# Performance work log

Hardware: AMD Instinct MI355X
Metric: run time of the kernel (lower is better)

## Reference

```python
import jax, jax.numpy as jnp
import numpy as np

N = 12288       # number of edge-triangle incidences
D_IN = 2        # input_dim
D_K = 8         # d_k
H1 = 32
H2 = 16
N_EDGES = 6144  # number of segments for scatter_softmax
N_TRI = 4096


def _layernorm(x, g, b, eps=1e-5):
    mu = jnp.mean(x, axis=-1, keepdims=True)
    var = jnp.mean((x - mu) ** 2, axis=-1, keepdims=True)
    return (x - mu) / jnp.sqrt(var + eps) * g + b


def _rmsnorm(x, w, eps=1e-6):
    rms = jnp.sqrt(jnp.mean(x ** 2, axis=-1, keepdims=True))
    return x / (rms + eps) * w


def setup_inputs() -> dict:
    key = jax.random.key(0)
    ks = jax.random.split(key, 16)

    def lin(k, out_d, in_d):
        k1, k2 = jax.random.split(k)
        bound = 1.0 / np.sqrt(in_d)
        W = jax.random.uniform(k1, (out_d, in_d), jnp.float32, -bound, bound)
        b = jax.random.uniform(k2, (out_d,), jnp.float32, -bound, bound)
        return W, b

    Wq, bq = lin(ks[0], D_K, D_IN)
    Wk, bk = lin(ks[1], D_K, D_IN)
    Wv, bv = lin(ks[2], D_K, D_IN)
    W1, b1 = lin(ks[3], H1, D_K)    # Linear(d_k, 32)
    Wr, br = lin(ks[4], H1, H1)     # ResBlock Linear(32, 32)
    W2, b2 = lin(ks[5], H2, H1)     # Linear(32, 16)
    W3, b3 = lin(ks[6], 1, H2)      # Linear(16, 1)

    return {
        "edge_features": jax.random.normal(ks[7], (N, D_IN), jnp.float32),
        "edge_ids_all": jax.random.randint(ks[8], (N,), 0, N_EDGES, jnp.int32),
        "triangle_ids_all": jax.random.randint(ks[9], (N,), 0, N_TRI, jnp.int32),
        "Wq": Wq, "bq": bq, "Wk": Wk, "bk": bk, "Wv": Wv, "bv": bv,
        "W1": W1, "b1": b1,
        "ln1_g": jnp.ones((H1,), jnp.float32), "ln1_b": jnp.zeros((H1,), jnp.float32),
        "rms_w": jnp.ones((H1,), jnp.float32),
        "Wr": Wr, "br": br,
        "ln2_g": jnp.ones((H1,), jnp.float32), "ln2_b": jnp.zeros((H1,), jnp.float32),
        "W2": W2, "b2": b2, "W3": W3, "b3": b3,
    }


def reference(edge_features, edge_ids_all, triangle_ids_all,
              Wq, bq, Wk, bk, Wv, bv,
              W1, b1, ln1_g, ln1_b, rms_w, Wr, br, ln2_g, ln2_b,
              W2, b2, W3, b3):
    q = edge_features @ Wq.T + bq          # [N, d_k]
    k = edge_features @ Wk.T + bk
    v = edge_features @ Wv.T + bv

    scores = (q @ k.T) / np.sqrt(D_K).astype(np.float32)   # [N, N]
    mask = triangle_ids_all[:, None] == triangle_ids_all[None, :]
    scores = jnp.where(mask, scores, -jnp.inf)
    attn = jax.nn.softmax(scores, axis=1)                   # row softmax
    attended = attn @ v                                     # [N, d_k]

    # attention_mlp
    h = _layernorm(attended @ W1.T + b1, ln1_g, ln1_b)
    h = jax.nn.gelu(h, approximate=False)
    h = h + jax.nn.relu(_rmsnorm(h, rms_w) @ Wr.T + br)     # ResBlock
    h = _layernorm(h, ln2_g, ln2_b)
    h = jax.nn.gelu(h @ W2.T + b2, approximate=False)
    logits = (h @ W3.T + b3)[:, 0]                          # [N]

    # scatter_softmax over edge_ids segments
    seg_max = jax.ops.segment_max(logits, edge_ids_all, num_segments=N_EDGES)
    seg_max = jnp.where(jnp.isfinite(seg_max), seg_max, 0.0)
    e = jnp.exp(logits - seg_max[edge_ids_all])
    seg_sum = jax.ops.segment_sum(e, edge_ids_all, num_segments=N_EDGES)
    weights = e / seg_sum[edge_ids_all]
    return weights
```

## Files before the change

### kernel.cpp

```cpp
#include <hip/hip_runtime.h>
#include <math.h>

#define N_INC   12288
#define N_EDGES 6144
#define N_TRI   4096

__device__ __forceinline__ unsigned enc_f(float f) {
    int b = __float_as_int(f);
    return (b >= 0) ? (unsigned(b) | 0x80000000u) : ~unsigned(b);
}
__device__ __forceinline__ float dec_f(unsigned u) {
    int b = (u & 0x80000000u) ? int(u & 0x7FFFFFFFu) : int(~u);
    return __int_as_float(b);
}

__device__ __forceinline__ float gelu_exact(float x) {
    return 0.5f * x * (1.0f + erff(x * 0.70710678118654752f));
}

__global__ void k_qkv(const float* __restrict__ ef, const int* __restrict__ tri,
                      const float* __restrict__ Wq, const float* __restrict__ bq,
                      const float* __restrict__ Wk, const float* __restrict__ bk,
                      const float* __restrict__ Wv, const float* __restrict__ bv,
                      float* __restrict__ q, float* __restrict__ k, float* __restrict__ v,
                      int* __restrict__ counts) {
    int i = blockIdx.x * blockDim.x + threadIdx.x;
    if (i >= N_INC) return;
    float x0 = ef[i * 2], x1 = ef[i * 2 + 1];
#pragma unroll
    for (int d = 0; d < 8; d++) {
        q[i * 8 + d] = Wq[d * 2] * x0 + Wq[d * 2 + 1] * x1 + bq[d];
        k[i * 8 + d] = Wk[d * 2] * x0 + Wk[d * 2 + 1] * x1 + bk[d];
        v[i * 8 + d] = Wv[d * 2] * x0 + Wv[d * 2 + 1] * x1 + bv[d];
    }
    atomicAdd(&counts[tri[i]], 1);
}

__global__ void k_scan(const int* __restrict__ counts,
                       int* __restrict__ offsets, int* __restrict__ cursor) {
    __shared__ int lds[1024];
    int t = threadIdx.x;
    int c0 = counts[t * 4 + 0], c1 = counts[t * 4 + 1];
    int c2 = counts[t * 4 + 2], c3 = counts[t * 4 + 3];
    int s = c0 + c1 + c2 + c3;
    lds[t] = s;
    __syncthreads();
    for (int off = 1; off < 1024; off <<= 1) {
        int val = (t >= off) ? lds[t - off] : 0;
        __syncthreads();
        lds[t] += val;
        __syncthreads();
    }
    int base = lds[t] - s;
    int o0 = base, o1 = base + c0, o2 = o1 + c1, o3 = o2 + c2;
    offsets[t * 4 + 0] = o0; offsets[t * 4 + 1] = o1;
    offsets[t * 4 + 2] = o2; offsets[t * 4 + 3] = o3;
    cursor[t * 4 + 0] = o0;  cursor[t * 4 + 1] = o1;
    cursor[t * 4 + 2] = o2;  cursor[t * 4 + 3] = o3;
    if (t == 1023) offsets[4096] = lds[1023];
}

__global__ void k_fill(const int* __restrict__ tri, int* __restrict__ cursor,
                       int* __restrict__ list) {
    int i = blockIdx.x * blockDim.x + threadIdx.x;
    if (i >= N_INC) return;
    int pos = atomicAdd(&cursor[tri[i]], 1);
    list[pos] = i;
}

__global__ void __launch_bounds__(64)
k_main(const float* __restrict__ q, const float* __restrict__ k, const float* __restrict__ v,
       const int* __restrict__ tri, const int* __restrict__ eid,
       const int* __restrict__ offsets, const int* __restrict__ list,
       const float* __restrict__ W1, const float* __restrict__ b1,
       const float* __restrict__ ln1g, const float* __restrict__ ln1b,
       const float* __restrict__ rmsw,
       const float* __restrict__ Wr, const float* __restrict__ br,
       const float* __restrict__ ln2g, const float* __restrict__ ln2b,
       const float* __restrict__ W2, const float* __restrict__ b2,
       const float* __restrict__ W3, const float* __restrict__ b3,
       float* __restrict__ logits, unsigned* __restrict__ segmax) {
    int i = blockIdx.x * blockDim.x + threadIdx.x;
    if (i >= N_INC) return;

    float qi[8];
#pragma unroll
    for (int d = 0; d < 8; d++) qi[d] = q[i * 8 + d];

    int t = tri[i];
    int s0 = offsets[t], s1 = offsets[t + 1];

    float m = -1e30f, l = 0.f, acc[8];
#pragma unroll
    for (int d = 0; d < 8; d++) acc[d] = 0.f;

    for (int p = s0; p < s1; p++) {
        int j = list[p];
        float sc = 0.f;
#pragma unroll
        for (int d = 0; d < 8; d++) sc += qi[d] * k[j * 8 + d];
        sc *= 0.35355339059327373f;
        float nm = fmaxf(m, sc);
        float scale = expf(m - nm);
        float w = expf(sc - nm);
        l = l * scale + w;
#pragma unroll
        for (int d = 0; d < 8; d++) acc[d] = acc[d] * scale + w * v[j * 8 + d];
        m = nm;
    }
    float inv_l = 1.f / l;
    float att[8];
#pragma unroll
    for (int d = 0; d < 8; d++) att[d] = acc[d] * inv_l;

    float h[32];
#pragma unroll
    for (int o = 0; o < 32; o++) {
        float a = b1[o];
#pragma unroll
        for (int d = 0; d < 8; d++) a += W1[o * 8 + d] * att[d];
        h[o] = a;
    }
    {
        float mu = 0.f;
#pragma unroll
        for (int o = 0; o < 32; o++) mu += h[o];
        mu *= (1.f / 32.f);
        float var = 0.f;
#pragma unroll
        for (int o = 0; o < 32; o++) { float d = h[o] - mu; var += d * d; }
        var *= (1.f / 32.f);
        float is = 1.f / sqrtf(var + 1e-5f);
#pragma unroll
        for (int o = 0; o < 32; o++) h[o] = (h[o] - mu) * is * ln1g[o] + ln1b[o];
    }
#pragma unroll
    for (int o = 0; o < 32; o++) h[o] = gelu_exact(h[o]);
    {
        float ss = 0.f;
#pragma unroll
        for (int o = 0; o < 32; o++) ss += h[o] * h[o];
        float rms = sqrtf(ss * (1.f / 32.f));
        float ir = 1.f / (rms + 1e-6f);
        float hn[32];
#pragma unroll
        for (int o = 0; o < 32; o++) hn[o] = h[o] * ir * rmsw[o];
#pragma unroll
        for (int o = 0; o < 32; o++) {
            float a = br[o];
#pragma unroll
            for (int in = 0; in < 32; in++) a += Wr[o * 32 + in] * hn[in];
            h[o] += fmaxf(a, 0.f);
        }
    }
    {
        float mu = 0.f;
#pragma unroll
        for (int o = 0; o < 32; o++) mu += h[o];
        mu *= (1.f / 32.f);
        float var = 0.f;
#pragma unroll
        for (int o = 0; o < 32; o++) { float d = h[o] - mu; var += d * d; }
        var *= (1.f / 32.f);
        float is = 1.f / sqrtf(var + 1e-5f);
#pragma unroll
        for (int o = 0; o < 32; o++) h[o] = (h[o] - mu) * is * ln2g[o] + ln2b[o];
    }
    float h2[16];
#pragma unroll
    for (int o = 0; o < 16; o++) {
        float a = b2[o];
#pragma unroll
        for (int in = 0; in < 32; in++) a += W2[o * 32 + in] * h[in];
        h2[o] = gelu_exact(a);
    }
    float lg = b3[0];
#pragma unroll
    for (int in = 0; in < 16; in++) lg += W3[in] * h2[in];

    logits[i] = lg;
    atomicMax(&segmax[eid[i]], enc_f(lg));
}

__global__ void k_exp(const float* __restrict__ logits, const int* __restrict__ eid,
                      const unsigned* __restrict__ segmax, float* __restrict__ ebuf,
                      float* __restrict__ segsum) {
    int i = blockIdx.x * blockDim.x + threadIdx.x;
    if (i >= N_INC) return;
    float sm = dec_f(segmax[eid[i]]);
    float ex = expf(logits[i] - sm);
    ebuf[i] = ex;
    atomicAdd(&segsum[eid[i]], ex);
}

__global__ void k_final(const float* __restrict__ ebuf, const int* __restrict__ eid,
                        const float* __restrict__ segsum, float* __restrict__ out) {
    int i = blockIdx.x * blockDim.x + threadIdx.x;
    if (i >= N_INC) return;
    out[i] = ebuf[i] / segsum[eid[i]];
}

extern "C" void kernel_launch(void* const* d_in, const int* in_sizes, int n_in,
                              void* d_out, int out_size, void* d_ws, size_t ws_size,
                              hipStream_t stream) {
    const float* ef   = (const float*)d_in[0];
    const int*   eid  = (const int*)d_in[1];
    const int*   tri  = (const int*)d_in[2];
    const float* Wq   = (const float*)d_in[3];  const float* bq = (const float*)d_in[4];
    const float* Wk   = (const float*)d_in[5];  const float* bk = (const float*)d_in[6];
    const float* Wv   = (const float*)d_in[7];  const float* bv = (const float*)d_in[8];
    const float* W1   = (const float*)d_in[9];  const float* b1 = (const float*)d_in[10];
    const float* ln1g = (const float*)d_in[11]; const float* ln1b = (const float*)d_in[12];
    const float* rmsw = (const float*)d_in[13];
    const float* Wr   = (const float*)d_in[14]; const float* br = (const float*)d_in[15];
    const float* ln2g = (const float*)d_in[16]; const float* ln2b = (const float*)d_in[17];
    const float* W2   = (const float*)d_in[18]; const float* b2 = (const float*)d_in[19];
    const float* W3   = (const float*)d_in[20]; const float* b3 = (const float*)d_in[21];

    float* ws     = (float*)d_ws;
    float* q      = ws;
    float* kk     = q + N_INC * 8;
    float* vv     = kk + N_INC * 8;
    float* logits = vv + N_INC * 8;
    float* ebuf   = logits + N_INC;
    float* segsum = ebuf + N_INC;
    unsigned* segmax = (unsigned*)(segsum + N_EDGES);
    int* counts   = (int*)(segmax + N_EDGES);
    int* offsets  = counts + N_TRI;
    int* cursor   = offsets + N_TRI + 1;
    int* list     = cursor + N_TRI;

    hipMemsetAsync(segsum, 0, (size_t)(2 * N_EDGES + N_TRI) * sizeof(int), stream);

    const int B = 256;
    const int G = (N_INC + B - 1) / B;

    k_qkv<<<G, B, 0, stream>>>(ef, tri, Wq, bq, Wk, bk, Wv, bv, q, kk, vv, counts);
    k_scan<<<1, 1024, 0, stream>>>(counts, offsets, cursor);
    k_fill<<<G, B, 0, stream>>>(tri, cursor, list);
    k_main<<<(N_INC + 63) / 64, 64, 0, stream>>>(q, kk, vv, tri, eid, offsets, list,
                                                 W1, b1, ln1g, ln1b, rmsw, Wr, br,
                                                 ln2g, ln2b, W2, b2, W3, b3,
                                                 logits, segmax);
    k_exp<<<G, B, 0, stream>>>(logits, eid, segmax, ebuf, segsum);
    k_final<<<G, B, 0, stream>>>(ebuf, eid, segsum, (float*)d_out);
}
```

Before: 144.5 us.

## Fuse pipeline into one cooperative kernel with fixed-capacity triangle/edge buckets

Replaces the six-kernel pipeline (QKV, scan, fill, main, exp, final) plus memset with a single cooperative kernel that uses grid-wide syncs between phases. The prefix-scan CSR build is replaced by fixed-capacity buckets per triangle and per edge, filled with atomics. The scatter softmax becomes a per-edge gather pass, which removes the atomicMax and atomicAdd passes. This cuts launch overhead and intermediate buffers. The trade-offs are grid-sync cost, fewer CUs in use (48 blocks), and silent truncation if any segment exceeds the bucket capacity.

```diff
diff --git a/kernel.cpp b/kernel.cpp
--- a/kernel.cpp
+++ b/kernel.cpp
@@ -1,247 +1,199 @@
 #include <hip/hip_runtime.h>
+#include <hip/hip_cooperative_groups.h>
 #include <math.h>
+
+namespace cg = cooperative_groups;
 
 #define N_INC   12288
 #define N_EDGES 6144
 #define N_TRI   4096
+#define CAP_T   32
+#define CAP_E   16
+#define BLK     256
+#define GRD     48
 
-__device__ __forceinline__ unsigned enc_f(float f) {
-    int b = __float_as_int(f);
-    return (b >= 0) ? (unsigned(b) | 0x80000000u) : ~unsigned(b);
-}
-__device__ __forceinline__ float dec_f(unsigned u) {
-    int b = (u & 0x80000000u) ? int(u & 0x7FFFFFFFu) : int(~u);
-    return __int_as_float(b);
-}
+struct Params {
+    const float* ef; const int* eid; const int* tri;
+    const float *Wq, *bq, *Wk, *bk, *Wv, *bv;
+    const float *W1, *b1, *ln1g, *ln1b, *rmsw, *Wr, *br, *ln2g, *ln2b, *W2, *b2, *W3, *b3;
+    float* out;
+    float *kbuf, *vbuf, *logits;
+    int *tri_cnt, *tri_bkt, *edge_cnt, *edge_bkt;
+};
 
 __device__ __forceinline__ float gelu_exact(float x) {
     return 0.5f * x * (1.0f + erff(x * 0.70710678118654752f));
 }
 
-__global__ void k_qkv(const float* __restrict__ ef, const int* __restrict__ tri,
-                      const float* __restrict__ Wq, const float* __restrict__ bq,
-                      const float* __restrict__ Wk, const float* __restrict__ bk,
-                      const float* __restrict__ Wv, const float* __restrict__ bv,
-                      float* __restrict__ q, float* __restrict__ k, float* __restrict__ v,
-                      int* __restrict__ counts) {
-    int i = blockIdx.x * blockDim.x + threadIdx.x;
-    if (i >= N_INC) return;
-    float x0 = ef[i * 2], x1 = ef[i * 2 + 1];
-#pragma unroll
-    for (int d = 0; d < 8; d++) {
-        q[i * 8 + d] = Wq[d * 2] * x0 + Wq[d * 2 + 1] * x1 + bq[d];
-        k[i * 8 + d] = Wk[d * 2] * x0 + Wk[d * 2 + 1] * x1 + bk[d];
-        v[i * 8 + d] = Wv[d * 2] * x0 + Wv[d * 2 + 1] * x1 + bv[d];
-    }
-    atomicAdd(&counts[tri[i]], 1);
-}
+__global__ void __launch_bounds__(BLK)
+fused_kernel(Params p) {
+    cg::grid_group grid = cg::this_grid();
+    const int gid = blockIdx.x * BLK + threadIdx.x;
 
-__global__ void k_scan(const int* __restrict__ counts,
-                       int* __restrict__ offsets, int* __restrict__ cursor) {
-    __shared__ int lds[1024];
-    int t = threadIdx.x;
-    int c0 = counts[t * 4 + 0], c1 = counts[t * 4 + 1];
-    int c2 = counts[t * 4 + 2], c3 = counts[t * 4 + 3];
-    int s = c0 + c1 + c2 + c3;
-    lds[t] = s;
-    __syncthreads();
-    for (int off = 1; off < 1024; off <<= 1) {
-        int val = (t >= off) ? lds[t - off] : 0;
-        __syncthreads();
-        lds[t] += val;
-        __syncthreads();
-    }
-    int base = lds[t] - s;
-    int o0 = base, o1 = base + c0, o2 = o1 + c1, o3 = o2 + c2;
-    offsets[t * 4 + 0] = o0; offsets[t * 4 + 1] = o1;
-    offsets[t * 4 + 2] = o2; offsets[t * 4 + 3] = o3;
-    cursor[t * 4 + 0] = o0;  cursor[t * 4 + 1] = o1;
-    cursor[t * 4 + 2] = o2;  cursor[t * 4 + 3] = o3;
-    if (t == 1023) offsets[4096] = lds[1023];
-}
-
-__global__ void k_fill(const int* __restrict__ tri, int* __restrict__ cursor,
-                       int* __restrict__ list) {
-    int i = blockIdx.x * blockDim.x + threadIdx.x;
-    if (i >= N_INC) return;
-    int pos = atomicAdd(&cursor[tri[i]], 1);
-    list[pos] = i;
-}
-
-__global__ void __launch_bounds__(64)
-k_main(const float* __restrict__ q, const float* __restrict__ k, const float* __restrict__ v,
-       const int* __restrict__ tri, const int* __restrict__ eid,
-       const int* __restrict__ offsets, const int* __restrict__ list,
-       const float* __restrict__ W1, const float* __restrict__ b1,
-       const float* __restrict__ ln1g, const float* __restrict__ ln1b,
-       const float* __restrict__ rmsw,
-       const float* __restrict__ Wr, const float* __restrict__ br,
-       const float* __restrict__ ln2g, const float* __restrict__ ln2b,
-       const float* __restrict__ W2, const float* __restrict__ b2,
-       const float* __restrict__ W3, const float* __restrict__ b3,
-       float* __restrict__ logits, unsigned* __restrict__ segmax) {
-    int i = blockIdx.x * blockDim.x + threadIdx.x;
-    if (i >= N_INC) return;
+    if (gid < N_TRI)   p.tri_cnt[gid]  = 0;
+    if (gid < N_EDGES) p.edge_cnt[gid] = 0;
+    grid.sync();
 
     float qi[8];
+    if (gid < N_INC) {
+        float x0 = p.ef[gid * 2], x1 = p.ef[gid * 2 + 1];
 #pragma unroll
-    for (int d = 0; d < 8; d++) qi[d] = q[i * 8 + d];
+        for (int d = 0; d < 8; d++) {
+            qi[d]               = p.Wq[d * 2] * x0 + p.Wq[d * 2 + 1] * x1 + p.bq[d];
+            p.kbuf[gid * 8 + d] = p.Wk[d * 2] * x0 + p.Wk[d * 2 + 1] * x1 + p.bk[d];
+            p.vbuf[gid * 8 + d] = p.Wv[d * 2] * x0 + p.Wv[d * 2 + 1] * x1 + p.bv[d];
+        }
+        int t = p.tri[gid];
+        int s = atomicAdd(&p.tri_cnt[t], 1);
+        if (s < CAP_T) p.tri_bkt[t * CAP_T + s] = gid;
+        int e = p.eid[gid];
+        s = atomicAdd(&p.edge_cnt[e], 1);
+        if (s < CAP_E) p.edge_bkt[e * CAP_E + s] = gid;
+    }
+    grid.sync();
 
-    int t = tri[i];
-    int s0 = offsets[t], s1 = offsets[t + 1];
+    if (gid < N_INC) {
+        int t = p.tri[gid];
+        int n = min(p.tri_cnt[t], CAP_T);
 
-    float m = -1e30f, l = 0.f, acc[8];
+        float m = -1e30f, l = 0.f, acc[8];
 #pragma unroll
-    for (int d = 0; d < 8; d++) acc[d] = 0.f;
+        for (int d = 0; d < 8; d++) acc[d] = 0.f;
 
-    for (int p = s0; p < s1; p++) {
-        int j = list[p];
-        float sc = 0.f;
+        for (int s = 0; s < n; s++) {
+            int j = p.tri_bkt[t * CAP_T + s];
+            float sc = 0.f;
 #pragma unroll
-        for (int d = 0; d < 8; d++) sc += qi[d] * k[j * 8 + d];
-        sc *= 0.35355339059327373f;
-        float nm = fmaxf(m, sc);
-        float scale = expf(m - nm);
-        float w = expf(sc - nm);
-        l = l * scale + w;
+            for (int d = 0; d < 8; d++) sc += qi[d] * p.kbuf[j * 8 + d];
+            sc *= 0.35355339059327373f;
+            float nm = fmaxf(m, sc);
+            float scale = expf(m - nm);
+            float w = expf(sc - nm);
+            l = l * scale + w;
 #pragma unroll
-        for (int d = 0; d < 8; d++) acc[d] = acc[d] * scale + w * v[j * 8 + d];
-        m = nm;
-    }
-    float inv_l = 1.f / l;
-    float att[8];
+            for (int d = 0; d < 8; d++) acc[d] = acc[d] * scale + w * p.vbuf[j * 8 + d];
+            m = nm;
+        }
+        float inv_l = 1.f / l;
+        float att[8];
 #pragma unroll
-    for (int d = 0; d < 8; d++) att[d] = acc[d] * inv_l;
+        for (int d = 0; d < 8; d++) att[d] = acc[d] * inv_l;
 
-    float h[32];
-#pragma unroll
-    for (int o = 0; o < 32; o++) {
-        float a = b1[o];
-#pragma unroll
-        for (int d = 0; d < 8; d++) a += W1[o * 8 + d] * att[d];
-        h[o] = a;
-    }
-    {
-        float mu = 0.f;
-#pragma unroll
-        for (int o = 0; o < 32; o++) mu += h[o];
-        mu *= (1.f / 32.f);
-        float var = 0.f;
-#pragma unroll
-        for (int o = 0; o < 32; o++) { float d = h[o] - mu; var += d * d; }
-        var *= (1.f / 32.f);
-        float is = 1.f / sqrtf(var + 1e-5f);
-#pragma unroll
-        for (int o = 0; o < 32; o++) h[o] = (h[o] - mu) * is * ln1g[o] + ln1b[o];
-    }
-#pragma unroll
-    for (int o = 0; o < 32; o++) h[o] = gelu_exact(h[o]);
-    {
-        float ss = 0.f;
-#pragma unroll
-        for (int o = 0; o < 32; o++) ss += h[o] * h[o];
-        float rms = sqrtf(ss * (1.f / 32.f));
-        float ir = 1.f / (rms + 1e-6f);
-        float hn[32];
-#pragma unroll
-        for (int o = 0; o < 32; o++) hn[o] = h[o] * ir * rmsw[o];
+        float h[32];
 #pragma unroll
         for (int o = 0; o < 32; o++) {
-            float a = br[o];
+            float a = p.b1[o];
 #pragma unroll
-            for (int in = 0; in < 32; in++) a += Wr[o * 32 + in] * hn[in];
-            h[o] += fmaxf(a, 0.f);
+            for (int d = 0; d < 8; d++) a += p.W1[o * 8 + d] * att[d];
+            h[o] = a;
+        }
+        {
+            float mu = 0.f;
+#pragma unroll
+            for (int o = 0; o < 32; o++) mu += h[o];
+            mu *= (1.f / 32.f);
+            float var = 0.f;
+#pragma unroll
+            for (int o = 0; o < 32; o++) { float d = h[o] - mu; var += d * d; }
+            var *= (1.f / 32.f);
+            float is = 1.f / sqrtf(var + 1e-5f);
+#pragma unroll
+            for (int o = 0; o < 32; o++) h[o] = (h[o] - mu) * is * p.ln1g[o] + p.ln1b[o];
+        }
+#pragma unroll
+        for (int o = 0; o < 32; o++) h[o] = gelu_exact(h[o]);
+        {
+            float ss = 0.f;
+#pragma unroll
+            for (int o = 0; o < 32; o++) ss += h[o] * h[o];
+            float rms = sqrtf(ss * (1.f / 32.f));
+            float ir = 1.f / (rms + 1e-6f);
+            float hn[32];
+#pragma unroll
+            for (int o = 0; o < 32; o++) hn[o] = h[o] * ir * p.rmsw[o];
+#pragma unroll
+            for (int o = 0; o < 32; o++) {
+                float a = p.br[o];
+#pragma unroll
+                for (int in = 0; in < 32; in++) a += p.Wr[o * 32 + in] * hn[in];
+                h[o] += fmaxf(a, 0.f);
+            }
+        }
+        {
+            float mu = 0.f;
+#pragma unroll
+            for (int o = 0; o < 32; o++) mu += h[o];
+            mu *= (1.f / 32.f);
+            float var = 0.f;
+#pragma unroll
+            for (int o = 0; o < 32; o++) { float d = h[o] - mu; var += d * d; }
+            var *= (1.f / 32.f);
+            float is = 1.f / sqrtf(var + 1e-5f);
+#pragma unroll
+            for (int o = 0; o < 32; o++) h[o] = (h[o] - mu) * is * p.ln2g[o] + p.ln2b[o];
+        }
+        float h2[16];
+#pragma unroll
+        for (int o = 0; o < 16; o++) {
+            float a = p.b2[o];
+#pragma unroll
+            for (int in = 0; in < 32; in++) a += p.W2[o * 32 + in] * h[in];
+            h2[o] = gelu_exact(a);
+        }
+        float lg = p.b3[0];
+#pragma unroll
+        for (int in = 0; in < 16; in++) lg += p.W3[in] * h2[in];
+
+        p.logits[gid] = lg;
+    }
+    grid.sync();
+
+    if (gid < N_EDGES) {
+        int n = min(p.edge_cnt[gid], CAP_E);
+        if (n > 0) {
+            const int* bkt = &p.edge_bkt[gid * CAP_E];
+            float mx = -1e30f;
+            for (int s = 0; s < n; s++) mx = fmaxf(mx, p.logits[bkt[s]]);
+            float sum = 0.f;
+            for (int s = 0; s < n; s++) sum += expf(p.logits[bkt[s]] - mx);
+            float inv = 1.f / sum;
+            for (int s = 0; s < n; s++) {
+                int idx = bkt[s];
+                p.out[idx] = expf(p.logits[idx] - mx) * inv;
+            }
         }
     }
-    {
-        float mu = 0.f;
-#pragma unroll
-        for (int o = 0; o < 32; o++) mu += h[o];
-        mu *= (1.f / 32.f);
-        float var = 0.f;
-#pragma unroll
-        for (int o = 0; o < 32; o++) { float d = h[o] - mu; var += d * d; }
-        var *= (1.f / 32.f);
-        float is = 1.f / sqrtf(var + 1e-5f);
-#pragma unroll
-        for (int o = 0; o < 32; o++) h[o] = (h[o] - mu) * is * ln2g[o] + ln2b[o];
-    }
-    float h2[16];
-#pragma unroll
-    for (int o = 0; o < 16; o++) {
-        float a = b2[o];
-#pragma unroll
-        for (int in = 0; in < 32; in++) a += W2[o * 32 + in] * h[in];
-        h2[o] = gelu_exact(a);
-    }
-    float lg = b3[0];
-#pragma unroll
-    for (int in = 0; in < 16; in++) lg += W3[in] * h2[in];
-
-    logits[i] = lg;
-    atomicMax(&segmax[eid[i]], enc_f(lg));
-}
-
-__global__ void k_exp(const float* __restrict__ logits, const int* __restrict__ eid,
-                      const unsigned* __restrict__ segmax, float* __restrict__ ebuf,
-                      float* __restrict__ segsum) {
-    int i = blockIdx.x * blockDim.x + threadIdx.x;
-    if (i >= N_INC) return;
-    float sm = dec_f(segmax[eid[i]]);
-    float ex = expf(logits[i] - sm);
-    ebuf[i] = ex;
-    atomicAdd(&segsum[eid[i]], ex);
-}
-
-__global__ void k_final(const float* __restrict__ ebuf, const int* __restrict__ eid,
-                        const float* __restrict__ segsum, float* __restrict__ out) {
-    int i = blockIdx.x * blockDim.x + threadIdx.x;
-    if (i >= N_INC) return;
-    out[i] = ebuf[i] / segsum[eid[i]];
 }
 
 extern "C" void kernel_launch(void* const* d_in, const int* in_sizes, int n_in,
                               void* d_out, int out_size, void* d_ws, size_t ws_size,
                               hipStream_t stream) {
-    const float* ef   = (const float*)d_in[0];
-    const int*   eid  = (const int*)d_in[1];
-    const int*   tri  = (const int*)d_in[2];
-    const float* Wq   = (const float*)d_in[3];  const float* bq = (const float*)d_in[4];
-    const float* Wk   = (const float*)d_in[5];  const float* bk = (const float*)d_in[6];
-    const float* Wv   = (const float*)d_in[7];  const float* bv = (const float*)d_in[8];
-    const float* W1   = (const float*)d_in[9];  const float* b1 = (const float*)d_in[10];
-    const float* ln1g = (const float*)d_in[11]; const float* ln1b = (const float*)d_in[12];
-    const float* rmsw = (const float*)d_in[13];
-    const float* Wr   = (const float*)d_in[14]; const float* br = (const float*)d_in[15];
-    const float* ln2g = (const float*)d_in[16]; const float* ln2b = (const float*)d_in[17];
-    const float* W2   = (const float*)d_in[18]; const float* b2 = (const float*)d_in[19];
-    const float* W3   = (const float*)d_in[20]; const float* b3 = (const float*)d_in[21];
+    Params p;
+    p.ef   = (const float*)d_in[0];
+    p.eid  = (const int*)d_in[1];
+    p.tri  = (const int*)d_in[2];
+    p.Wq   = (const float*)d_in[3];  p.bq   = (const float*)d_in[4];
+    p.Wk   = (const float*)d_in[5];  p.bk   = (const float*)d_in[6];
+    p.Wv   = (const float*)d_in[7];  p.bv   = (const float*)d_in[8];
+    p.W1   = (const float*)d_in[9];  p.b1   = (const float*)d_in[10];
+    p.ln1g = (const float*)d_in[11]; p.ln1b = (const float*)d_in[12];
+    p.rmsw = (const float*)d_in[13];
+    p.Wr   = (const float*)d_in[14]; p.br   = (const float*)d_in[15];
+    p.ln2g = (const float*)d_in[16]; p.ln2b = (const float*)d_in[17];
+    p.W2   = (const float*)d_in[18]; p.b2   = (const float*)d_in[19];
+    p.W3   = (const float*)d_in[20]; p.b3   = (const float*)d_in[21];
+    p.out  = (float*)d_out;
 
-    float* ws     = (float*)d_ws;
-    float* q      = ws;
-    float* kk     = q + N_INC * 8;
-    float* vv     = kk + N_INC * 8;
-    float* logits = vv + N_INC * 8;
-    float* ebuf   = logits + N_INC;
-    float* segsum = ebuf + N_INC;
-    unsigned* segmax = (unsigned*)(segsum + N_EDGES);
-    int* counts   = (int*)(segmax + N_EDGES);
-    int* offsets  = counts + N_TRI;
-    int* cursor   = offsets + N_TRI + 1;
-    int* list     = cursor + N_TRI;
+    float* ws  = (float*)d_ws;
+    p.kbuf     = ws;
+    p.vbuf     = p.kbuf + N_INC * 8;
+    p.logits   = p.vbuf + N_INC * 8;
+    p.tri_cnt  = (int*)(p.logits + N_INC);
+    p.tri_bkt  = p.tri_cnt + N_TRI;
+    p.edge_cnt = p.tri_bkt + N_TRI * CAP_T;
+    p.edge_bkt = p.edge_cnt + N_EDGES;
 
-    hipMemsetAsync(segsum, 0, (size_t)(2 * N_EDGES + N_TRI) * sizeof(int), stream);
-
-    const int B = 256;
-    const int G = (N_INC + B - 1) / B;
-
-    k_qkv<<<G, B, 0, stream>>>(ef, tri, Wq, bq, Wk, bk, Wv, bv, q, kk, vv, counts);
-    k_scan<<<1, 1024, 0, stream>>>(counts, offsets, cursor);
-    k_fill<<<G, B, 0, stream>>>(tri, cursor, list);
-    k_main<<<(N_INC + 63) / 64, 64, 0, stream>>>(q, kk, vv, tri, eid, offsets, list,
-                                                 W1, b1, ln1g, ln1b, rmsw, Wr, br,
-                                                 ln2g, ln2b, W2, b2, W3, b3,
-                                                 logits, segmax);
-    k_exp<<<G, B, 0, stream>>>(logits, eid, segmax, ebuf, segsum);
-    k_final<<<G, B, 0, stream>>>(ebuf, eid, segsum, (float*)d_out);
+    void* kargs[] = { (void*)&p };
+    hipLaunchCooperativeKernel((const void*)fused_kernel, dim3(GRD), dim3(BLK),
+                               kargs, 0, stream);
 }
```

After: 195.1 us. +35.0%, slower.
